# Optimization experiments

Measured on AMD Instinct MI355X. Metric: run time of the kernel, lower is better.

## Reference

```python
import jax, jax.numpy as jnp
import numpy as np

HUMAN_SIZE = 54
NUM_ACTIONS = 15
INPUT_SIZE = HUMAN_SIZE + NUM_ACTIONS  # 69
RNN_SIZE = 2048
BATCH = 512
SRC_LEN = 100
TGT_LEN = 50


def setup_inputs() -> dict:
    key = jax.random.key(0)
    ks = jax.random.split(key, 8)
    s = 1.0 / np.sqrt(RNN_SIZE)
    return {
        "encoder_inputs": jax.random.normal(ks[0], (BATCH, SRC_LEN, INPUT_SIZE), jnp.float32),
        "decoder_inputs": jax.random.normal(ks[1], (BATCH, TGT_LEN, INPUT_SIZE), jnp.float32),
        # GRUCell params (torch layout: weight_ih [3H, D], weight_hh [3H, H])
        "W_ih": jax.random.uniform(ks[2], (3 * RNN_SIZE, INPUT_SIZE), jnp.float32, -s, s),
        "W_hh": jax.random.uniform(ks[3], (3 * RNN_SIZE, RNN_SIZE), jnp.float32, -s, s),
        "b_ih": jax.random.uniform(ks[4], (3 * RNN_SIZE,), jnp.float32, -s, s),
        "b_hh": jax.random.uniform(ks[5], (3 * RNN_SIZE,), jnp.float32, -s, s),
        # fc1: Linear(rnn_size -> input_size)
        "fc1_w": jax.random.uniform(ks[6], (INPUT_SIZE, RNN_SIZE), jnp.float32, -s, s),
        "fc1_b": jax.random.uniform(ks[7], (INPUT_SIZE,), jnp.float32, -s, s),
    }


def _gru_cell(x, h, W_ih, W_hh, b_ih, b_hh):
    # torch.nn.GRUCell math
    gi = x @ W_ih.T + b_ih  # [B, 3H]
    gh = h @ W_hh.T + b_hh  # [B, 3H]
    i_r, i_z, i_n = jnp.split(gi, 3, axis=-1)
    h_r, h_z, h_n = jnp.split(gh, 3, axis=-1)
    r = jax.nn.sigmoid(i_r + h_r)
    z = jax.nn.sigmoid(i_z + h_z)
    n = jnp.tanh(i_n + r * h_n)
    return (1.0 - z) * n + z * h


def reference(encoder_inputs, decoder_inputs, W_ih, W_hh, b_ih, b_hh, fc1_w, fc1_b):
    B = encoder_inputs.shape[0]
    state0 = jnp.zeros((B, RNN_SIZE), encoder_inputs.dtype)

    # Encoder: source_seq_len - 1 steps (dropout p=0.0 -> identity)
    enc_t = jnp.swapaxes(encoder_inputs[:, : SRC_LEN - 1], 0, 1)  # [L-1, B, D]

    def enc_step(h, x):
        return _gru_cell(x, h, W_ih, W_hh, b_ih, b_hh), None

    state, _ = jax.lax.scan(enc_step, state0, enc_t)

    # (loop_function feeds the previous output back as the next input).
    def dec_step(carry, _):
        h, inp = carry
        inp = jax.lax.stop_gradient(inp)  # inp.detach() in torch
        h = _gru_cell(inp, h, W_ih, W_hh, b_ih, b_hh)
        out = inp + h @ fc1_w.T + fc1_b  # residual
        return (h, out), out

    (_, _), outs = jax.lax.scan(dec_step, (state, decoder_inputs[:, 0]), None, length=TGT_LEN)
    return jnp.swapaxes(outs, 0, 1)  # [B, TGT_LEN, INPUT_SIZE]
```

## Files before the change

kernel.cpp:

```cpp
#include <hip/hip_runtime.h>

#define KP   2176
#define H    2048
#define IN   69
#define TGT  50
#define NKT  68

typedef unsigned short ushort_t;
typedef unsigned int   uint_t;
typedef __attribute__((ext_vector_type(8))) short  short8;
typedef __attribute__((ext_vector_type(4))) float  float4_t;

#define MFMA_BF16 __builtin_amdgcn_mfma_f32_16x16x32_bf16

__device__ __forceinline__ ushort_t f2bf(float f) {
  union { float f; unsigned u; } v; v.f = f;
  unsigned u = v.u;
  return (ushort_t)((u + 0x7fffu + ((u >> 16) & 1u)) >> 16);
}

template <int N> __device__ __forceinline__ void waitv() {
  asm volatile("s_waitcnt vmcnt(%0)" :: "n"(N) : "memory");
}
#define LGKM0() asm volatile("s_waitcnt lgkmcnt(0)" ::: "memory")
#define SGB0()  __builtin_amdgcn_sched_barrier(0)
#define FENCE() asm volatile("" ::: "memory")

template <int OFF> __device__ __forceinline__ void gld(short8& d, uint_t voff, const void* base) {
  asm volatile("global_load_dwordx4 %0, %1, %2 offset:%3"
               : "=v"(d) : "v"(voff), "s"(base), "n"(OFF));
}
template <int OFF> __device__ __forceinline__ void gld_sc(short8& d, uint_t voff, const void* base) {
  asm volatile("global_load_dwordx4 %0, %1, %2 offset:%3 sc0 sc1"
               : "=v"(d) : "v"(voff), "s"(base), "n"(OFF));
}
__device__ __forceinline__ void st128_sc(void* addr, short8 v) {
  asm volatile("global_store_dwordx4 %0, %1, off sc0 sc1" :: "v"(addr), "v"(v) : "memory");
}
__device__ __forceinline__ void st16_sc(void* addr, uint_t v) {
  asm volatile("global_store_short %0, %1, off sc0 sc1" :: "v"(addr), "v"(v) : "memory");
}
__device__ __forceinline__ void st32_sc(void* addr, float v) {
  asm volatile("global_store_dword %0, %1, off sc0 sc1" :: "v"(addr), "v"(v) : "memory");
}
__device__ __forceinline__ void ld32_sc_nw(float& d, const void* addr) {
  asm volatile("global_load_dword %0, %1, off sc0 sc1" : "=v"(d) : "v"(addr) : "memory");
}

__global__ void build_w3(const float* __restrict__ Whh, const float* __restrict__ Wih,
                         ushort_t* __restrict__ W3) {
  int i = blockIdx.x * 256 + threadIdx.x;
  int lane = i & 63;
  int kt = (i >> 6) % NKT;
  int rb = i / (64 * NKT);
  int cb = rb / 3, g = rb - cb * 3;
  int c  = cb * 16 + (lane & 15);
  int gr = g * H + c;
  int k0 = kt * 32 + (lane >> 4) * 8;
  short8 v;
  #pragma unroll
  for (int j = 0; j < 8; ++j) {
    int k = k0 + j;
    float val = 0.f;
    if (k < H) val = Whh[(size_t)gr * H + k];
    else if (k < H + IN) val = Wih[(size_t)gr * IN + (k - H)];
    v[j] = (short)f2bf(val);
  }
  *(short8*)(W3 + (size_t)i * 8) = v;
}

__global__ void build_f2(const float* __restrict__ fc1w, ushort_t* __restrict__ F2) {
  int i = blockIdx.x * 256 + threadIdx.x;
  int lane = i & 63;
  int ni = (i >> 6) % 5;
  int kt = i / 320;
  int j  = ni * 16 + (lane & 15);
  int k0 = kt * 32 + (lane >> 4) * 8;
  short8 v;
  #pragma unroll
  for (int jj = 0; jj < 8; ++jj) {
    float val = (j < IN) ? fc1w[(size_t)j * H + k0 + jj] : 0.f;
    v[jj] = (short)f2bf(val);
  }
  *(short8*)(F2 + (size_t)i * 8) = v;
}

__global__ void zero_u4(uint4* p, int n) {
  int i = blockIdx.x * 256 + threadIdx.x;
  if (i < n) p[i] = make_uint4(0, 0, 0, 0);
}

__device__ __forceinline__ size_t a2_x_off(int b, int j) {
  int k = 2048 + j;
  int kt = k >> 5, kk = k & 31;
  int mb = b >> 4;
  int ln = (b & 15) | ((kk >> 3) << 4);
  return ((size_t)(mb * NKT + kt) * 64 + ln) * 16 + (kk & 7) * 2;
}

__global__ void fill_x0(const float* __restrict__ enc, char* __restrict__ A2) {
  int i = blockIdx.x * 256 + threadIdx.x;
  int b = i / IN, j = i - b * IN;
  *(ushort_t*)(A2 + a2_x_off(b, j)) = f2bf(enc[(size_t)b * 100 * IN + j]);
}

__global__ __launch_bounds__(256, 1) void persist(
    const char* __restrict__ W3p, char* A0, char* A1, const char* __restrict__ F2p,
    const float* __restrict__ enc, const float* __restrict__ dec,
    const float* __restrict__ bih, const float* __restrict__ bhh,
    const float* __restrict__ fc1b, float* __restrict__ out, int* barcnt)
{
  __shared__ __align__(16) char ldsraw[25600];
  short8  (*Aring)[4][64] = (short8 (*)[4][64])ldsraw;
  ushort_t (*smh)[72]     = (ushort_t (*)[72])(ldsraw + 16384);

  const int tid = threadIdx.x;
  const int bid = blockIdx.x;
  const int lane = tid & 63, w = tid >> 6;
  const int l15 = lane & 15, l4 = lane >> 4;
  const int cg = (bid & 7) * 4 + ((bid >> 3) & 3);
  const int mt = bid >> 5;
  const int cb = cg * 4 + w;
  const int c  = cb * 16 + l15;

  const float br  = bih[c] + bhh[c];
  const float bz  = bih[H + c] + bhh[H + c];
  const float bin = bih[2 * H + c];
  const float bhn = bhh[2 * H + c];
  asm volatile("" :: "v"(br), "v"(bz), "v"(bin), "v"(bhn));

  float hreg[4][4] = {};

  const uint_t vAi  = (uint_t)(w * (NKT * 1024) + lane * 16);
  const uint_t vB0i = (uint_t)((cb * 3 + 0) * (NKT * 1024) + lane * 16);
  const uint_t vB1i = vB0i + (uint_t)(NKT * 1024);
  const uint_t vB2i = vB1i + (uint_t)(NKT * 1024);

  int epoch = 0;
  auto gbar = [&]() {
    asm volatile("s_waitcnt vmcnt(0) lgkmcnt(0)" ::: "memory");
    __builtin_amdgcn_s_barrier();
    ++epoch;
    if (tid == 0) {
      atomicAdd(barcnt, 1);
      const int tgt = epoch * 256;
      int v = 0;
      for (int it = 0; it < 20000000; ++it) {
        asm volatile("global_load_dword %0, %1, off sc0 sc1\n\ts_waitcnt vmcnt(0)"
                     : "=v"(v) : "v"((const int*)barcnt) : "memory");
        if (v >= tgt) break;
        __builtin_amdgcn_s_sleep(2);
      }
    }
    __builtin_amdgcn_s_barrier();
  };

  #pragma unroll 1
  for (int t = 0; t < 149; ++t) {
    char* Ain  = (t & 1) ? A1 : A0;
    char* Aout = (t & 1) ? A0 : A1;
    const void* ApW = Ain + (size_t)(mt * 4) * (NKT * 1024);

    uint_t vA = vAi;
    uint_t vB0 = vB0i, vB1 = vB1i, vB2 = vB2i;

    short8 sa[4], fb[8][3];
    short8 fa0, fa1, fa2, fa3;
    float4_t acc[4][4] = {};

#define AISS(sl) { gld_sc<0>(sa[sl], vA, ApW); vA += 1024; }
#define BISS(sl) { gld<0>(fb[sl][0], vB0, W3p); gld<0>(fb[sl][1], vB1, W3p); \
                   gld<0>(fb[sl][2], vB2, W3p); vB0 += 1024; vB1 += 1024; vB2 += 1024; }
#define MFMA3(mi, fav, j, G2) \
  acc[mi][0]  = MFMA_BF16(fav, fb[j][0], acc[mi][0], 0, 0, 0); \
  acc[mi][1]  = MFMA_BF16(fav, fb[j][1], acc[mi][1], 0, 0, 0); \
  acc[mi][G2] = MFMA_BF16(fav, fb[j][2], acc[mi][G2], 0, 0, 0);
#define MFMA12(j, G2) MFMA3(0, fa0, j, G2) MFMA3(1, fa1, j, G2) \
                      MFMA3(2, fa2, j, G2) MFMA3(3, fa3, j, G2)
#define RDFA(ss) \
  FENCE(); \
  fa0 = Aring[ss][0][lane]; fa1 = Aring[ss][1][lane]; \
  fa2 = Aring[ss][2][lane]; fa3 = Aring[ss][3][lane];
#define GRUT(u, G2) \
  AISS((u + 4) & 3) BISS((u + 7) & 7) \
  waitv<15>(); SGB0(); \
  Aring[(u + 1) & 3][w][lane] = sa[(u + 1) & 3]; \
  LGKM0(); \
  __builtin_amdgcn_s_barrier(); \
  RDFA(u & 3) \
  LGKM0(); SGB0(); \
  MFMA12(u, G2)
#define GRUTA(u, NW) \
  AISS((u + 4) & 3) \
  waitv<NW>(); SGB0(); \
  Aring[(u + 1) & 3][w][lane] = sa[(u + 1) & 3]; \
  LGKM0(); \
  __builtin_amdgcn_s_barrier(); \
  RDFA(u & 3) \
  LGKM0(); SGB0(); \
  MFMA12(u, 2)
#define GRUTN_W(u, NW, G2) \
  waitv<NW>(); SGB0(); \
  Aring[(u + 1) & 3][w][lane] = sa[(u + 1) & 3]; \
  LGKM0(); \
  __builtin_amdgcn_s_barrier(); \
  RDFA(u & 3) \
  LGKM0(); SGB0(); \
  MFMA12(u, G2)
#define GRUTN_NW(u, NW, G2) \
  waitv<NW>(); SGB0(); \
  LGKM0(); \
  __builtin_amdgcn_s_barrier(); \
  RDFA(u & 3) \
  LGKM0(); SGB0(); \
  MFMA12(u, G2)

    AISS(0) AISS(1) AISS(2) AISS(3)
    BISS(0) BISS(1) BISS(2) BISS(3) BISS(4) BISS(5) BISS(6)
    waitv<24>(); SGB0();
    Aring[0][w][lane] = sa[0];
    LGKM0();
    __builtin_amdgcn_s_barrier();

    #pragma unroll 1
    for (int g8 = 0; g8 < 7; ++g8) {
      GRUT(0, 2) GRUT(1, 2) GRUT(2, 2) GRUT(3, 2)
      GRUT(4, 2) GRUT(5, 2) GRUT(6, 2) GRUT(7, 2)
    }
    GRUT(0, 2) GRUT(1, 2) GRUT(2, 2) GRUT(3, 2) GRUT(4, 2)
    GRUTA(5, 12) GRUTA(6, 9) GRUTA(7, 6)
    GRUTN_W(0, 2, 3) GRUTN_W(1, 1, 3) GRUTN_W(2, 0, 3) GRUTN_NW(3, 0, 3)

    #pragma unroll
    for (int mi = 0; mi < 4; ++mi) {
      #pragma unroll
      for (int r4 = 0; r4 < 4; ++r4) {
        float rg = 1.f / (1.f + __expf(-(acc[mi][0][r4] + br)));
        float zg = 1.f / (1.f + __expf(-(acc[mi][1][r4] + bz)));
        float ng = tanhf(acc[mi][3][r4] + bin + rg * (acc[mi][2][r4] + bhn));
        float hn = (1.f - zg) * ng + zg * hreg[mi][r4];
        hreg[mi][r4] = hn;
        smh[mi * 16 + l4 * 4 + r4][w * 16 + l15] = f2bf(hn);
      }
    }
    __syncthreads();
    #pragma unroll
    for (int e = 0; e < 2; ++e) {
      int cid = tid * 2 + e;
      int m = cid >> 3, ktrel = (cid >> 2) & 1, khi = cid & 3;
      short8 v = *(const short8*)&smh[m][ktrel * 32 + khi * 8];
      int m_abs = mt * 64 + m;
      int mb2 = m_abs >> 4;
      int ln = (m_abs & 15) | (khi << 4);
      int kt = cg * 2 + ktrel;
      st128_sc(Aout + ((size_t)(mb2 * NKT + kt) * 64 + ln) * 16, v);
    }
    if ((bid & 31) == 0 && t < 99) {
      const float* xs = (t < 98) ? (enc + (size_t)(t + 1) * IN) : dec;
      const int xstride = (t < 98) ? 100 * IN : TGT * IN;
      for (int i = tid; i < 64 * IN; i += 256) {
        int rr = i / IN, cc = i - rr * IN;
        int m = mt * 64 + rr;
        st16_sc(Aout + a2_x_off(m, cc), (uint_t)f2bf(xs[(size_t)m * xstride + cc]));
      }
    }
    gbar();

    if (t >= 99) {
      if (bid < 32) {
        const int d = t - 99;
        const int mbo = bid;
        float4_t* redf = (float4_t*)ldsraw;
        const void* F2b = (const char*)F2p + 4096;
        uint_t voA = (uint_t)((mbo * NKT + w * 16) * 1024 + lane * 16);
        uint_t vf  = (uint_t)((w * 16) * 5120 + lane * 16);
        short8 da[8], db[8][5];
        float4_t oa[5] = {};

#define DPRO(sl) \
        gld_sc<0>(da[sl], voA, Aout); \
        gld<0>(db[sl][0], vf, F2p); gld<1024>(db[sl][1], vf, F2p); \
        gld<2048>(db[sl][2], vf, F2p); gld<3072>(db[sl][3], vf, F2p); \
        gld<0>(db[sl][4], vf, F2b); \
        voA += 1024; vf += 5120;
#define DMM(sl) \
        { _Pragma("unroll") for (int nf = 0; nf < 5; ++nf) \
            oa[nf] = MFMA_BF16(da[sl], db[sl][nf], oa[nf], 0, 0, 0); }

        DPRO(0) DPRO(1) DPRO(2) DPRO(3) DPRO(4) DPRO(5) DPRO(6) DPRO(7)
        waitv<42>(); SGB0(); DMM(0) DPRO(0)
        waitv<42>(); SGB0(); DMM(1) DPRO(1)
        waitv<42>(); SGB0(); DMM(2) DPRO(2)
        waitv<42>(); SGB0(); DMM(3) DPRO(3)
        waitv<42>(); SGB0(); DMM(4) DPRO(4)
        waitv<42>(); SGB0(); DMM(5) DPRO(5)
        waitv<42>(); SGB0(); DMM(6) DPRO(6)
        waitv<42>(); SGB0(); DMM(7) DPRO(7)
        waitv<42>(); SGB0(); DMM(0)
        waitv<36>(); SGB0(); DMM(1)
        waitv<30>(); SGB0(); DMM(2)
        waitv<24>(); SGB0(); DMM(3)
        waitv<18>(); SGB0(); DMM(4)
        waitv<12>(); SGB0(); DMM(5)
        waitv<6>();  SGB0(); DMM(6)
        waitv<0>();  SGB0(); DMM(7)

        #pragma unroll
        for (int nf = 0; nf < 5; ++nf) redf[(w * 5 + nf) * 64 + lane] = oa[nf];
        __syncthreads();

        #pragma unroll 1
        for (int pass = 0; pass < 2; ++pass) {
          if (pass == 1 && w != 0) break;
          const int nf = pass ? 4 : w;
          float4_t sum = redf[(0 * 5 + nf) * 64 + lane] + redf[(1 * 5 + nf) * 64 + lane]
                       + redf[(2 * 5 + nf) * 64 + lane] + redf[(3 * 5 + nf) * 64 + lane];
          int j = nf * 16 + l15;
          if (j < IN) {
            float bj = fc1b[j];
            float iv0, iv1, iv2, iv3;
            if (d == 0) {
              iv0 = dec[(size_t)(mbo * 16 + l4 * 4 + 0) * (TGT * IN) + j];
              iv1 = dec[(size_t)(mbo * 16 + l4 * 4 + 1) * (TGT * IN) + j];
              iv2 = dec[(size_t)(mbo * 16 + l4 * 4 + 2) * (TGT * IN) + j];
              iv3 = dec[(size_t)(mbo * 16 + l4 * 4 + 3) * (TGT * IN) + j];
            } else {
              const float* pv = out + (size_t)(d - 1) * IN + j;
              ld32_sc_nw(iv0, pv + (size_t)(mbo * 16 + l4 * 4 + 0) * (TGT * IN));
              ld32_sc_nw(iv1, pv + (size_t)(mbo * 16 + l4 * 4 + 1) * (TGT * IN));
              ld32_sc_nw(iv2, pv + (size_t)(mbo * 16 + l4 * 4 + 2) * (TGT * IN));
              ld32_sc_nw(iv3, pv + (size_t)(mbo * 16 + l4 * 4 + 3) * (TGT * IN));
              waitv<0>(); SGB0();
            }
            float ivv[4] = {iv0, iv1, iv2, iv3};
            #pragma unroll
            for (int r4 = 0; r4 < 4; ++r4) {
              int m = mbo * 16 + l4 * 4 + r4;
              float v = sum[r4] + bj + ivv[r4];
              st32_sc(out + (size_t)m * (TGT * IN) + (size_t)d * IN + j, v);
              st16_sc(Aout + a2_x_off(m, j), (uint_t)f2bf(v));
            }
          }
        }
      }
      gbar();
    }
  }
}

extern "C" void kernel_launch(void* const* d_in, const int* in_sizes, int n_in,
                              void* d_out, int out_size, void* d_ws, size_t ws_size,
                              hipStream_t stream) {
  const float* enc  = (const float*)d_in[0];
  const float* dec  = (const float*)d_in[1];
  const float* Wih  = (const float*)d_in[2];
  const float* Whh  = (const float*)d_in[3];
  const float* b_ih = (const float*)d_in[4];
  const float* b_hh = (const float*)d_in[5];
  const float* fc1w = (const float*)d_in[6];
  const float* fc1b = (const float*)d_in[7];
  float* out = (float*)d_out;

  char* ws = (char*)d_ws;
  ushort_t* W3  = (ushort_t*)ws;
  char*     A0  = ws + 26738688;
  char*     A1  = ws + 28966912;
  int*      bar = (int*)(ws + 31195136);
  ushort_t* F2  = (ushort_t*)(ws + 31196160);

  build_w3<<<6528, 256, 0, stream>>>(Whh, Wih, W3);
  zero_u4<<<1089, 256, 0, stream>>>((uint4*)A0, 278592);
  fill_x0<<<138, 256, 0, stream>>>(enc, A0);
  build_f2<<<80, 256, 0, stream>>>(fc1w, F2);

  persist<<<256, 256, 0, stream>>>((const char*)W3, A0, A1, (const char*)F2,
                                   enc, dec, b_ih, b_hh, fc1b, out, bar);
}
```

Measured before the change: 4.307 ms.

## Pair K-tiles per LDS barrier with 8-deep A ring and move hidden state to LDS

The GRU K-loop now processes two K-tiles per workgroup barrier, with an 8-slot A ring and deeper load prefetch, which halves the number of s_barrier syncs per step. The hidden-state accumulator moves from registers into LDS to free VGPRs for the larger prefetch buffers. The grid-barrier spin sleep is also shortened. The trade-off is more LDS use, an extra LDS read and write per element in the epilogue, and a bigger VGPR footprint for the in-flight loads.

```diff
diff --git a/kernel.cpp b/kernel.cpp
--- a/kernel.cpp
+++ b/kernel.cpp
@@ -25,6 +25,7 @@
 #define LGKM0() asm volatile("s_waitcnt lgkmcnt(0)" ::: "memory")
 #define SGB0()  __builtin_amdgcn_sched_barrier(0)
 #define FENCE() asm volatile("" ::: "memory")
+#define BARR()  __builtin_amdgcn_s_barrier()
 
 template <int OFF> __device__ __forceinline__ void gld(short8& d, uint_t voff, const void* base) {
   asm volatile("global_load_dwordx4 %0, %1, %2 offset:%3"
@@ -110,9 +111,10 @@
     const float* __restrict__ bih, const float* __restrict__ bhh,
     const float* __restrict__ fc1b, float* __restrict__ out, int* barcnt)
 {
-  __shared__ __align__(16) char ldsraw[25600];
+  __shared__ __align__(16) char ldsraw[58368];
   short8  (*Aring)[4][64] = (short8 (*)[4][64])ldsraw;
-  ushort_t (*smh)[72]     = (ushort_t (*)[72])(ldsraw + 16384);
+  ushort_t (*smh)[72]     = (ushort_t (*)[72])(ldsraw + 32768);
+  float*   hregL          = (float*)(ldsraw + 41984);
 
   const int tid = threadIdx.x;
   const int bid = blockIdx.x;
@@ -129,7 +131,8 @@
   const float bhn = bhh[2 * H + c];
   asm volatile("" :: "v"(br), "v"(bz), "v"(bin), "v"(bhn));
 
-  float hreg[4][4] = {};
+  #pragma unroll
+  for (int k = 0; k < 16; ++k) hregL[k * 256 + tid] = 0.f;
 
   const uint_t vAi  = (uint_t)(w * (NKT * 1024) + lane * 16);
   const uint_t vB0i = (uint_t)((cb * 3 + 0) * (NKT * 1024) + lane * 16);
@@ -139,7 +142,7 @@
   int epoch = 0;
   auto gbar = [&]() {
     asm volatile("s_waitcnt vmcnt(0) lgkmcnt(0)" ::: "memory");
-    __builtin_amdgcn_s_barrier();
+    BARR();
     ++epoch;
     if (tid == 0) {
       atomicAdd(barcnt, 1);
@@ -149,10 +152,10 @@
         asm volatile("global_load_dword %0, %1, off sc0 sc1\n\ts_waitcnt vmcnt(0)"
                      : "=v"(v) : "v"((const int*)barcnt) : "memory");
         if (v >= tgt) break;
-        __builtin_amdgcn_s_sleep(2);
+        __builtin_amdgcn_s_sleep(1);
       }
     }
-    __builtin_amdgcn_s_barrier();
+    BARR();
   };
 
   #pragma unroll 1
@@ -164,72 +167,74 @@
     uint_t vA = vAi;
     uint_t vB0 = vB0i, vB1 = vB1i, vB2 = vB2i;
 
-    short8 sa[4], fb[8][3];
+    short8 sa[8], fb[8][3];
     short8 fa0, fa1, fa2, fa3;
     float4_t acc[4][4] = {};
 
 #define AISS(sl) { gld_sc<0>(sa[sl], vA, ApW); vA += 1024; }
 #define BISS(sl) { gld<0>(fb[sl][0], vB0, W3p); gld<0>(fb[sl][1], vB1, W3p); \
                    gld<0>(fb[sl][2], vB2, W3p); vB0 += 1024; vB1 += 1024; vB2 += 1024; }
-#define MFMA3(mi, fav, j, G2) \
+#define MFMA3F(mi, fav, j, G2) \
   acc[mi][0]  = MFMA_BF16(fav, fb[j][0], acc[mi][0], 0, 0, 0); \
   acc[mi][1]  = MFMA_BF16(fav, fb[j][1], acc[mi][1], 0, 0, 0); \
   acc[mi][G2] = MFMA_BF16(fav, fb[j][2], acc[mi][G2], 0, 0, 0);
-#define MFMA12(j, G2) MFMA3(0, fa0, j, G2) MFMA3(1, fa1, j, G2) \
-                      MFMA3(2, fa2, j, G2) MFMA3(3, fa3, j, G2)
-#define RDFA(ss) \
-  FENCE(); \
+#define MFMA12A(j, G2) MFMA3F(0, fa0, j, G2) MFMA3F(1, fa1, j, G2) \
+                       MFMA3F(2, fa2, j, G2) MFMA3F(3, fa3, j, G2)
+#define AWR(s) Aring[s][w][lane] = sa[s];
+#define RD1(ss) \
   fa0 = Aring[ss][0][lane]; fa1 = Aring[ss][1][lane]; \
   fa2 = Aring[ss][2][lane]; fa3 = Aring[ss][3][lane];
-#define GRUT(u, G2) \
-  AISS((u + 4) & 3) BISS((u + 7) & 7) \
-  waitv<15>(); SGB0(); \
-  Aring[(u + 1) & 3][w][lane] = sa[(u + 1) & 3]; \
+
+#define GPAIR(u, G2) \
+  AISS(2*(u)) AISS(2*(u)+1) \
+  BISS((2*(u)+6)&7) BISS((2*(u)+7)&7) \
+  waitv<24>(); SGB0(); \
+  AWR((2*(u)+2)&7) AWR((2*(u)+3)&7) \
   LGKM0(); \
-  __builtin_amdgcn_s_barrier(); \
-  RDFA(u & 3) \
+  BARR(); \
+  FENCE(); \
+  RD1(2*(u)) \
   LGKM0(); SGB0(); \
-  MFMA12(u, G2)
-#define GRUTA(u, NW) \
-  AISS((u + 4) & 3) \
-  waitv<NW>(); SGB0(); \
-  Aring[(u + 1) & 3][w][lane] = sa[(u + 1) & 3]; \
-  LGKM0(); \
-  __builtin_amdgcn_s_barrier(); \
-  RDFA(u & 3) \
+  MFMA12A(2*(u), G2) \
+  FENCE(); \
+  RD1(2*(u)+1) \
   LGKM0(); SGB0(); \
-  MFMA12(u, 2)
-#define GRUTN_W(u, NW, G2) \
-  waitv<NW>(); SGB0(); \
-  Aring[(u + 1) & 3][w][lane] = sa[(u + 1) & 3]; \
-  LGKM0(); \
-  __builtin_amdgcn_s_barrier(); \
-  RDFA(u & 3) \
-  LGKM0(); SGB0(); \
-  MFMA12(u, G2)
-#define GRUTN_NW(u, NW, G2) \
-  waitv<NW>(); SGB0(); \
-  LGKM0(); \
-  __builtin_amdgcn_s_barrier(); \
-  RDFA(u & 3) \
-  LGKM0(); SGB0(); \
-  MFMA12(u, G2)
-
-    AISS(0) AISS(1) AISS(2) AISS(3)
-    BISS(0) BISS(1) BISS(2) BISS(3) BISS(4) BISS(5) BISS(6)
+  MFMA12A(2*(u)+1, G2)
+
+    AISS(0) AISS(1)
+    AISS(2) AISS(3) BISS(0) BISS(1)
+    AISS(4) AISS(5) BISS(2) BISS(3)
+    AISS(6) AISS(7) BISS(4) BISS(5)
     waitv<24>(); SGB0();
-    Aring[0][w][lane] = sa[0];
+    AWR(0) AWR(1)
     LGKM0();
-    __builtin_amdgcn_s_barrier();
+    BARR();
 
     #pragma unroll 1
-    for (int g8 = 0; g8 < 7; ++g8) {
-      GRUT(0, 2) GRUT(1, 2) GRUT(2, 2) GRUT(3, 2)
-      GRUT(4, 2) GRUT(5, 2) GRUT(6, 2) GRUT(7, 2)
-    }
-    GRUT(0, 2) GRUT(1, 2) GRUT(2, 2) GRUT(3, 2) GRUT(4, 2)
-    GRUTA(5, 12) GRUTA(6, 9) GRUTA(7, 6)
-    GRUTN_W(0, 2, 3) GRUTN_W(1, 1, 3) GRUTN_W(2, 0, 3) GRUTN_NW(3, 0, 3)
+    for (int g4 = 0; g4 < 7; ++g4) {
+      GPAIR(0, 2) GPAIR(1, 2) GPAIR(2, 2) GPAIR(3, 2)
+    }
+    GPAIR(0, 2) GPAIR(1, 2)
+    BISS(2) BISS(3)
+    waitv<22>(); SGB0();
+    AWR(6) AWR(7)
+    LGKM0(); BARR(); FENCE();
+    RD1(4) LGKM0(); SGB0(); MFMA12A(4, 2)
+    FENCE(); RD1(5) LGKM0(); SGB0(); MFMA12A(5, 2)
+    waitv<14>(); SGB0();
+    AWR(0) AWR(1)
+    LGKM0(); BARR(); FENCE();
+    RD1(6) LGKM0(); SGB0(); MFMA12A(6, 2)
+    FENCE(); RD1(7) LGKM0(); SGB0(); MFMA12A(7, 2)
+    waitv<6>(); SGB0();
+    AWR(2) AWR(3)
+    LGKM0(); BARR(); FENCE();
+    RD1(0) LGKM0(); SGB0(); MFMA12A(0, 3)
+    FENCE(); RD1(1) LGKM0(); SGB0(); MFMA12A(1, 3)
+    waitv<0>(); SGB0();
+    LGKM0(); BARR(); FENCE();
+    RD1(2) LGKM0(); SGB0(); MFMA12A(2, 3)
+    FENCE(); RD1(3) LGKM0(); SGB0(); MFMA12A(3, 3)
 
     #pragma unroll
     for (int mi = 0; mi < 4; ++mi) {
@@ -238,8 +243,9 @@
         float rg = 1.f / (1.f + __expf(-(acc[mi][0][r4] + br)));
         float zg = 1.f / (1.f + __expf(-(acc[mi][1][r4] + bz)));
         float ng = tanhf(acc[mi][3][r4] + bin + rg * (acc[mi][2][r4] + bhn));
-        float hn = (1.f - zg) * ng + zg * hreg[mi][r4];
-        hreg[mi][r4] = hn;
+        float hold = hregL[(mi * 4 + r4) * 256 + tid];
+        float hn = (1.f - zg) * ng + zg * hold;
+        hregL[(mi * 4 + r4) * 256 + tid] = hn;
         smh[mi * 16 + l4 * 4 + r4][w * 16 + l15] = f2bf(hn);
       }
     }
```

After: 4.493 ms. +4.3%, slower.
